# Kernel optimization log

Measured on AMD Instinct MI355X. Metric: run time of the kernel, lower is better.

## Reference

```python
import jax, jax.numpy as jnp
import numpy as np

CD_STEPS = 1

def _sample_binary(p, u):
    # relu(sign(p - u)): 1.0 where p > u else 0.0
    return (p > u).astype(p.dtype)

def setup_inputs() -> dict:
    key = jax.random.key(0)
    k_v, k_w, k_vb, k_uh, k_uv = jax.random.split(key, 5)
    B, V, H = 8192, 2048, 1024
    return {
        "v": jax.random.uniform(k_v, (B, V), dtype=jnp.float32),
        "w": jax.random.normal(k_w, (V, H), dtype=jnp.float32) * 0.01,
        "vb": jax.random.normal(k_vb, (V,), dtype=jnp.float32) * 0.01,
        "hb": jnp.zeros((H,), dtype=jnp.float32),
        "u_h": jax.random.uniform(k_uh, (CD_STEPS + 1, B, H), dtype=jnp.float32),
        "u_v": jax.random.uniform(k_uv, (CD_STEPS, B, V), dtype=jnp.float32),
    }

def reference(v, w, vb, hb, u_h, u_v):
    sig = jax.nn.sigmoid
    # mean-field forward
    h_p = sig(hb + v @ w)                     # [B,H]
    h_prediction = h_p
    v_prediction = sig(vb + h_p @ w.T)        # [B,V]
    reconstruction_error = jnp.mean(jnp.mean(jnp.abs(v - v_prediction), axis=1))
    # data statistics
    h = _sample_binary(h_p, u_h[0])           # [B,H]
    vb_data_grad = jnp.sum(v, axis=0)
    hb_data_grad = jnp.sum(h_p, axis=0)
    # sum_b outer(v_b, h_b) == v^T @ h (original materialized [B,V,H])
    w_data_grad = jnp.einsum('bv,bh->vh', v, h)
    # CD-k chain
    vk = v
    for k in range(CD_STEPS):
        vk = _sample_binary(sig(vb + h @ w.T), u_v[k])
        h = _sample_binary(sig(hb + vk @ w), u_h[k + 1])
    vb_model_grad = jnp.sum(vk, axis=0)
    hb_model_grad = jnp.sum(h, axis=0)
    w_model_grad = jnp.einsum('bv,bh->vh', vk, h)
    vb_grad = vb_model_grad - vb_data_grad
    hb_grad = hb_model_grad - hb_data_grad
    w_grad = w_model_grad - w_data_grad
    return h_prediction, reconstruction_error, w_grad, vb_grad, hb_grad
```

## Files before the change

### kernel.cpp

```cpp
#include <hip/hip_runtime.h>


typedef unsigned short u16;
typedef unsigned char u8;
typedef short s16x8 __attribute__((ext_vector_type(8)));
typedef float f32x4 __attribute__((ext_vector_type(4)));
typedef int i32x4 __attribute__((ext_vector_type(4)));
typedef u16 u16x4 __attribute__((ext_vector_type(4)));
typedef u16 u16x8 __attribute__((ext_vector_type(8)));
typedef u8 u8x8 __attribute__((ext_vector_type(8)));

constexpr int Bn = 8192, Vn = 2048, Hn = 1024;
constexpr size_t VH = (size_t)Vn * Hn;
constexpr size_t BH = (size_t)Bn * Hn;
constexpr size_t OUT_RECON = BH;
constexpr size_t OUT_WGRAD = OUT_RECON + 1;
constexpr size_t OUT_VBG   = OUT_WGRAD + VH;
constexpr size_t OUT_HBG   = OUT_VBG + Vn;

__device__ __forceinline__ u16 f2bf(float x) {
  union { float f; unsigned u; } a; a.f = x;
  unsigned r = a.u + 0x7FFFu + ((a.u >> 16) & 1u);
  return (u16)(r >> 16);
}
__device__ __forceinline__ float bf2f(u16 h) {
  union { unsigned u; float f; } a; a.u = ((unsigned)h) << 16;
  return a.f;
}
__device__ __forceinline__ float sigmoidf_(float x) {
  return 1.0f / (1.0f + __expf(-x));
}

using gptr_t = const unsigned int __attribute__((address_space(1)))*;
using lptr_t = unsigned int __attribute__((address_space(3)))*;

__device__ __forceinline__ void gload16(const void* g, void* l) {
  __builtin_amdgcn_global_load_lds((gptr_t)(unsigned long long)g,
                                   (lptr_t)(unsigned long long)l, 16, 0, 0);
}

__global__ void prep_all_k(const float* __restrict__ v, u16* __restrict__ vcat,
                           u16* __restrict__ vT, float* __restrict__ vbd_p,
                           const float* __restrict__ w, u16* __restrict__ w_cat,
                           u16* __restrict__ wTc) {
  __shared__ u16 tile16[64][68];
  __shared__ float cs[16][64];
  __shared__ float tile32[64][65];
  const int bx = blockIdx.x;
  const int t = threadIdx.x;
  if (bx < 4096) {
    const int b0 = (bx & 127) << 6, c0 = (bx >> 7) << 6;
    const int rg = t >> 4;
    const int cg = (t & 15) << 2;
    float ca[4] = {0.f, 0.f, 0.f, 0.f};
#pragma unroll
    for (int i = 0; i < 4; ++i) {
      int r = rg + 16 * i;
      f32x4 x = *(const f32x4*)&v[(size_t)(b0 + r) * Vn + c0 + cg];
      u16x4 hi, lo;
#pragma unroll
      for (int j = 0; j < 4; ++j) {
        hi[j] = f2bf(x[j]);
        lo[j] = f2bf(x[j] - bf2f(hi[j]));
        tile16[r][cg + j] = hi[j];
        ca[j] += x[j];
      }
      *(u16x4*)&vcat[(size_t)(b0 + r) * (2 * Vn) + c0 + cg] = hi;
      *(u16x4*)&vcat[(size_t)(b0 + r) * (2 * Vn) + Vn + c0 + cg] = lo;
    }
#pragma unroll
    for (int j = 0; j < 4; ++j) cs[rg][cg + j] = ca[j];
    __syncthreads();
    if (t < 64) {
      float s = 0.f;
#pragma unroll
      for (int k = 0; k < 16; ++k) s += cs[k][t];
      vbd_p[(size_t)(bx & 127) * Vn + c0 + t] = s;
    }
#pragma unroll
    for (int s2 = 0; s2 < 2; ++s2) {
      int c = t >> 2;
      int seg = (t & 3) + 4 * s2;
      u16x8 pk;
#pragma unroll
      for (int i = 0; i < 8; ++i) pk[i] = tile16[seg * 8 + i][c];
      *(u16x8*)&vT[(size_t)(c0 + c) * Bn + b0 + seg * 8] = pk;
    }
  } else {
    const int wb = bx - 4096;
    const int v0 = (wb & 31) << 6, h0 = (wb >> 5) << 6;
    const int c = t & 63, r = t >> 6;
    for (int rr = r; rr < 64; rr += 4) {
      float x = w[(size_t)(v0 + rr) * Hn + h0 + c];
      tile32[rr][c] = x;
      u16 hi = f2bf(x), lo = f2bf(x - bf2f(hi));
      w_cat[(size_t)(v0 + rr) * (2 * Hn) + h0 + c]      = hi;
      w_cat[(size_t)(v0 + rr) * (2 * Hn) + Hn + h0 + c] = lo;
    }
    __syncthreads();
    for (int rr = r; rr < 64; rr += 4) {
      float x = tile32[c][rr];
      u16 hi = f2bf(x), lo = f2bf(x - bf2f(hi));
      size_t ro = (size_t)(h0 + rr) * (2 * Vn);
      wTc[ro + v0 + c]      = hi;
      wTc[ro + Vn + v0 + c] = lo;
    }
  }
}

template <int M>
__global__ void epi_h_k(const float* __restrict__ p0, const float* __restrict__ p1,
                        const float* __restrict__ bias, const float* __restrict__ uni,
                        float* __restrict__ f32out, u16* __restrict__ hp_out,
                        u16* __restrict__ hbin_out, u16* __restrict__ tout,
                        float* __restrict__ colp) {
  __shared__ u16 tile[64][68];
  __shared__ float cs[16][64];
  const int b0 = blockIdx.x * 64, c0 = blockIdx.y * 64;
  const int t = threadIdx.x;
  const int rg = t >> 4, cg = (t & 15) << 2;
  float ca[4] = {0.f, 0.f, 0.f, 0.f};
#pragma unroll
  for (int i = 0; i < 4; ++i) {
    int r = rg + 16 * i;
    size_t e = (size_t)(b0 + r) * Hn + c0 + cg;
    f32x4 a = *(const f32x4*)&p0[e];
    f32x4 b = *(const f32x4*)&p1[e];
    f32x4 uu = *(const f32x4*)&uni[e];
    f32x4 hpv;
    u16x4 hb16, qv;
#pragma unroll
    for (int j = 0; j < 4; ++j) {
      float hp = sigmoidf_(a[j] + b[j] + bias[c0 + cg + j]);
      u16 qb = (hp > uu[j]) ? (u16)0x3F80 : (u16)0;
      tile[r][cg + j] = qb;
      if constexpr (M == 1) {
        hpv[j] = hp; hb16[j] = f2bf(hp); qv[j] = qb;
        ca[j] += hp;
      } else {
        ca[j] += (qb ? 1.f : 0.f);
      }
    }
    if constexpr (M == 1) {
      *(f32x4*)&f32out[e] = hpv;
      *(u16x4*)&hp_out[e] = hb16;
      *(u16x4*)&hbin_out[e] = qv;
    }
  }
#pragma unroll
  for (int j = 0; j < 4; ++j) cs[rg][cg + j] = ca[j];
  __syncthreads();
  if (t < 64) {
    float s = 0.f;
#pragma unroll
    for (int k = 0; k < 16; ++k) s += cs[k][t];
    colp[(size_t)blockIdx.x * Hn + c0 + t] = s;
  }
  if constexpr (M == 5) {
    u8* tout8 = (u8*)tout;
#pragma unroll
    for (int s2 = 0; s2 < 2; ++s2) {
      int c = t >> 2;
      int seg = (t & 3) + 4 * s2;
      u8x8 pk;
#pragma unroll
      for (int i = 0; i < 8; ++i) pk[i] = tile[seg * 8 + i][c] ? (u8)1 : (u8)0;
      *(u8x8*)&tout8[(size_t)(c0 + c) * Bn + b0 + seg * 8] = pk;
    }
  } else {
#pragma unroll
    for (int s2 = 0; s2 < 2; ++s2) {
      int c = t >> 2;
      int seg = (t & 3) + 4 * s2;
      u16x8 pk;
#pragma unroll
      for (int i = 0; i < 8; ++i) pk[i] = tile[seg * 8 + i][c];
      *(u16x8*)&tout[(size_t)(c0 + c) * Bn + b0 + seg * 8] = pk;
    }
  }
}

template <int MODE>
__global__ __launch_bounds__(512) void gemm256(
    const u16* __restrict__ A, int lda, const u16* __restrict__ Bm, int ldb, int K,
    const float* __restrict__ bias, const float* __restrict__ uni,
    const float* __restrict__ aux, float* __restrict__ f32out,
    u16* __restrict__ bfout, const u16* __restrict__ aux16,
    float* __restrict__ redp, u16* __restrict__ tout, float* __restrict__ colp) {
  constexpr bool TRANS = (MODE == 4);
  __shared__ __align__(16) u16 smem[TRANS ? 67584 : 65536];
  const int t = threadIdx.x;
  const int lane = t & 63, wave = t >> 6;
  const int wr = (wave >> 2) << 7;
  const int wc = (wave & 3) << 6;
  int bidx = blockIdx.x, bidy = blockIdx.y, bidz = blockIdx.z;
  if constexpr (MODE == 3) {
    const int orig = blockIdx.x + (blockIdx.y << 3) + (blockIdx.z << 5);
    bidz = orig & 7;
    const int r = orig >> 3;
    bidx = r & 7;
    bidy = r >> 3;
  }
  const int bm = bidx << 8, bn = bidy << 8;
  int kbeg = 0;
  float* pout = f32out;
  if constexpr (MODE == 1 || MODE == 5) {
    kbeg = bidz * K;
    pout = (bidz == 0) ? f32out : redp;
  }
  if constexpr (MODE == 3) {
    size_t off = (size_t)bidz * (size_t)K;
    A += off;
    Bm += off;
    pout = ((bidz < 4) ? f32out : redp) + (size_t)(bidz & 3) * VH;
  }
  f32x4 acc[8][4] = {};
  const int sr = t >> 2;
  const int sc = (((t & 3) ^ ((t >> 3) & 3)) << 3);
  const u16* Ag  = A  + (size_t)(bm + sr) * lda + sc;
  const u16* Ag2 = Ag + (size_t)128 * lda;
  const u16* Bg  = Bm + (size_t)(bn + sr) * ldb + sc;
  const u16* Bg2 = Bg + (size_t)128 * ldb;
  const int fr = lane & 15, fg = lane >> 4;
  const int ga = ((fg ^ ((fr >> 1) & 3)) << 3);

  auto acolf = [&](int k0) -> int {
    if constexpr (MODE == 1)      return (k0 < 2048) ? k0 : k0 - 2048;
    else if constexpr (MODE == 4) return k0 & 1023;
    else if constexpr (MODE == 5) return k0 & 2047;
    else                          return k0;
  };
  auto bcolf = [&](int k0) -> int {
    if constexpr (MODE == 1) return (k0 < 4096) ? k0 : k0 - 4096;
    else                     return k0;
  };
  auto stageA = [&](int kt) {
    const int k0 = kbeg + (kt << 5);
    const int acol = acolf(k0);
    u16* ad = smem + (kt & 3) * 8192 + wave * 512;
    gload16(Ag + acol, ad);
    gload16(Ag2 + acol, ad + 4096);
  };
  auto stageB = [&](int kt) {
    const int k0 = kbeg + (kt << 5);
    const int bcol = bcolf(k0);
    u16* bd = smem + 32768 + (kt & 3) * 8192 + wave * 512;
    gload16(Bg + bcol, bd);
    gload16(Bg2 + bcol, bd + 4096);
  };
  auto pfl4 = [&](int ci) -> float {
    const int L = (ci << 9) + t;
    return uni[(size_t)(bm + (L >> 3)) * Vn + bn + ((L & 7) << 5)];
  };

  const int NT = K >> 5;
  const int pfbeg = NT - 8;
  stageA(0); stageB(0); stageA(1); stageB(1); stageA(2); stageB(2);
  asm volatile("s_waitcnt vmcnt(8)" ::: "memory");
  __builtin_amdgcn_s_barrier();
  asm volatile("" ::: "memory");
  s16x8 bf[4], af[4];
  for (int kt = 0; kt < NT; ++kt) {
    const int pb = kt & 3;
    const u16* Ab = smem + pb * 8192;
    const u16* Bb = smem + 32768 + pb * 8192;
    const bool st = (kt < NT - 3);
#pragma unroll
    for (int n = 0; n < 4; ++n)
      bf[n] = *(const s16x8*)&Bb[(wc + n * 16 + fr) * 32 + ga];
#pragma unroll
    for (int m = 0; m < 4; ++m)
      af[m] = *(const s16x8*)&Ab[(wr + m * 16 + fr) * 32 + ga];
    if (st) stageA(kt + 3);
    if constexpr (MODE == 4) {
      if (kt >= pfbeg && kt < pfbeg + 4) {
        float pfv = pfl4(kt - pfbeg);
        asm volatile("" :: "v"(pfv));
      }
    }
    __builtin_amdgcn_s_barrier();
    asm volatile("" ::: "memory");
    __builtin_amdgcn_s_setprio(1);
#pragma unroll
    for (int m = 0; m < 4; ++m)
#pragma unroll
      for (int n = 0; n < 4; ++n)
        acc[m][n] = __builtin_amdgcn_mfma_f32_16x16x32_bf16(af[m], bf[n], acc[m][n], 0, 0, 0);
    __builtin_amdgcn_s_setprio(0);
#pragma unroll
    for (int m = 0; m < 4; ++m)
      af[m] = *(const s16x8*)&Ab[(wr + (m + 4) * 16 + fr) * 32 + ga];
    if (st) stageB(kt + 3);
    if (kt < NT - 3) {
      asm volatile("s_waitcnt vmcnt(8)" ::: "memory");
    } else if (kt == NT - 3) {
      asm volatile("s_waitcnt vmcnt(4)" ::: "memory");
    } else if (kt == NT - 2) {
      asm volatile("s_waitcnt vmcnt(0)" ::: "memory");
    }
    __builtin_amdgcn_s_barrier();
    asm volatile("" ::: "memory");
    __builtin_amdgcn_s_setprio(1);
#pragma unroll
    for (int m = 0; m < 4; ++m)
#pragma unroll
      for (int n = 0; n < 4; ++n)
        acc[m + 4][n] = __builtin_amdgcn_mfma_f32_16x16x32_bf16(af[m], bf[n], acc[m + 4][n], 0, 0, 0);
    __builtin_amdgcn_s_setprio(0);
  }

  constexpr int NC = (MODE == 4) ? Vn : Hn;
  const int fq = lane >> 4;

  if constexpr (MODE == 1 || MODE == 3 || MODE == 5) {
#pragma unroll
    for (int m = 0; m < 8; ++m)
#pragma unroll
      for (int n = 0; n < 4; ++n)
#pragma unroll
        for (int j = 0; j < 4; ++j) {
          int rl = wr + m * 16 + fq * 4 + j;
          int cl = wc + n * 16 + fr;
          pout[(size_t)(bm + rl) * NC + bn + cl] = acc[m][n][j];
        }
  }

  if constexpr (MODE == 4) {
    __syncthreads();
    float bcol[4];
#pragma unroll
    for (int n = 0; n < 4; ++n) bcol[n] = bias[bn + wc + n * 16 + fr];
    const size_t ebase = (size_t)(bm + wr + fq * 4) * NC + (bn + wc + fr);
    float ux[8][4];
    auto ld4 = [&](int ci, float* dst) {
      size_t e0 = ebase + (size_t)((ci >> 2) << 4) * NC + ((ci & 3) << 4);
      dst[0] = uni[e0];          dst[1] = uni[e0 + NC];
      dst[2] = uni[e0 + 2 * NC]; dst[3] = uni[e0 + 3 * NC];
    };
#pragma unroll
    for (int ci = 0; ci < 8; ++ci) ld4(ci, ux[ci]);
#pragma unroll
    for (int m = 0; m < 8; ++m)
#pragma unroll
      for (int n = 0; n < 4; ++n)
#pragma unroll
        for (int j = 0; j < 4; ++j)
          acc[m][n][j] = sigmoidf_(acc[m][n][j] + bcol[n]);
    float csum[4] = {0.f, 0.f, 0.f, 0.f};
#pragma unroll
    for (int ci = 0; ci < 32; ++ci) {
      const int m = ci >> 2, n = ci & 3;
      const int rl = wr + m * 16 + fq * 4;
      const int cl = wc + n * 16 + fr;
#pragma unroll
      for (int j = 0; j < 4; ++j) {
        u16 qb = (acc[m][n][j] > ux[ci & 7][j]) ? (u16)0x3F80 : (u16)0;
        smem[(rl + j) * 264 + cl] = qb;
        csum[n] += (qb ? 1.f : 0.f);
      }
      if (ci < 24) ld4(ci + 8, ux[ci & 7]);
    }
#pragma unroll
    for (int n = 0; n < 4; ++n) {
      float s = csum[n];
      s += __shfl_xor(s, 16);
      s += __shfl_xor(s, 32);
      if (fq == 0)
        colp[(size_t)(blockIdx.x * 2 + (wr >> 7)) * NC + (bn + wc + n * 16 + fr)] = s;
    }
    __syncthreads();
#pragma unroll
    for (int it = 0; it < 16; ++it) {
      int id = t + (it << 9);
      int r = id >> 5;
      int c0 = (id & 31) << 3;
      u16x8 pk = *(const u16x8*)&smem[r * 264 + c0];
      *(u16x8*)&bfout[(size_t)(bm + r) * NC + bn + c0] = pk;
    }
    {
      u8* tout8 = (u8*)tout;
      const int c = t & 255;
      const int half = t >> 8;
#pragma unroll
      for (int i8_ = 0; i8_ < 16; ++i8_) {
        u8x8 pk;
#pragma unroll
        for (int i2 = 0; i2 < 8; ++i2)
          pk[i2] = smem[(half * 128 + i8_ * 8 + i2) * 264 + c] ? (u8)1 : (u8)0;
        *(u8x8*)&tout8[(size_t)(bn + c) * Bn + bm + half * 128 + i8_ * 8] = pk;
      }
    }
  }
}

__global__ __launch_bounds__(512) void gemm_i8_k(
    const u8* __restrict__ A, const u8* __restrict__ Bm,
    float* __restrict__ out0, float* __restrict__ out4) {
  __shared__ __align__(16) u8 smem[131072];
  const int t = threadIdx.x;
  const int lane = t & 63, wave = t >> 6;
  const int wr = (wave >> 2) << 7;
  const int wc = (wave & 3) << 6;
  const int orig = blockIdx.x + (blockIdx.y << 3) + (blockIdx.z << 5);
  const int bidz = orig & 7;
  const int rr = orig >> 3;
  const int bidx = rr & 7, bidy = rr >> 3;
  const int bm = bidx << 8, bn = bidy << 8;
  const int kbeg = bidz << 10;
  float* pout = ((bidz < 4) ? out0 : out4) + (size_t)(bidz & 3) * VH;
  i32x4 acc[8][4] = {};
  const int sr = t >> 2;
  const int sc = (((t & 3) ^ ((t >> 3) & 3)) << 4);
  const u8* Ag  = A  + (size_t)(bm + sr) * Bn + sc;
  const u8* Ag2 = Ag + (size_t)128 * Bn;
  const u8* Bg  = Bm + (size_t)(bn + sr) * Bn + sc;
  const u8* Bg2 = Bg + (size_t)128 * Bn;
  const int fr = lane & 15, fg = lane >> 4;
  const int ga = ((fg ^ ((fr >> 1) & 3)) << 4);

  auto stageA = [&](int kt) {
    u8* ad = smem + (kt & 3) * 16384 + wave * 1024;
    gload16(Ag + kbeg + (kt << 6), ad);
    gload16(Ag2 + kbeg + (kt << 6), ad + 8192);
  };
  auto stageB = [&](int kt) {
    u8* bd = smem + 65536 + (kt & 3) * 16384 + wave * 1024;
    gload16(Bg + kbeg + (kt << 6), bd);
    gload16(Bg2 + kbeg + (kt << 6), bd + 8192);
  };

  constexpr int NT = 16;
  stageA(0); stageB(0); stageA(1); stageB(1); stageA(2); stageB(2);
  asm volatile("s_waitcnt vmcnt(8)" ::: "memory");
  __builtin_amdgcn_s_barrier();
  asm volatile("" ::: "memory");
  i32x4 bf[4], af[4];
  for (int kt = 0; kt < NT; ++kt) {
    const u8* Ab = smem + (kt & 3) * 16384;
    const u8* Bb = smem + 65536 + (kt & 3) * 16384;
    const bool st = (kt < NT - 3);
#pragma unroll
    for (int n = 0; n < 4; ++n)
      bf[n] = *(const i32x4*)&Bb[(wc + n * 16 + fr) * 64 + ga];
#pragma unroll
    for (int m = 0; m < 4; ++m)
      af[m] = *(const i32x4*)&Ab[(wr + m * 16 + fr) * 64 + ga];
    if (st) stageA(kt + 3);
    __builtin_amdgcn_s_barrier();
    asm volatile("" ::: "memory");
    __builtin_amdgcn_s_setprio(1);
#pragma unroll
    for (int m = 0; m < 4; ++m)
#pragma unroll
      for (int n = 0; n < 4; ++n)
        acc[m][n] = __builtin_amdgcn_mfma_i32_16x16x64_i8(af[m], bf[n], acc[m][n], 0, 0, 0);
    __builtin_amdgcn_s_setprio(0);
#pragma unroll
    for (int m = 0; m < 4; ++m)
      af[m] = *(const i32x4*)&Ab[(wr + (m + 4) * 16 + fr) * 64 + ga];
    if (st) stageB(kt + 3);
    if (kt < NT - 3) {
      asm volatile("s_waitcnt vmcnt(8)" ::: "memory");
    } else if (kt == NT - 3) {
      asm volatile("s_waitcnt vmcnt(4)" ::: "memory");
    } else if (kt == NT - 2) {
      asm volatile("s_waitcnt vmcnt(0)" ::: "memory");
    }
    __builtin_amdgcn_s_barrier();
    asm volatile("" ::: "memory");
    __builtin_amdgcn_s_setprio(1);
#pragma unroll
    for (int m = 0; m < 4; ++m)
#pragma unroll
      for (int n = 0; n < 4; ++n)
        acc[m + 4][n] = __builtin_amdgcn_mfma_i32_16x16x64_i8(af[m], bf[n], acc[m + 4][n], 0, 0, 0);
    __builtin_amdgcn_s_setprio(0);
  }

  const int fq = lane >> 4;
#pragma unroll
  for (int m = 0; m < 8; ++m)
#pragma unroll
    for (int n = 0; n < 4; ++n)
#pragma unroll
      for (int j = 0; j < 4; ++j) {
        int rl = wr + m * 16 + fq * 4 + j;
        int cl = wc + n * 16 + fr;
        pout[(size_t)(bm + rl) * Hn + bn + cl] = (float)acc[m][n][j];
      }
}

__global__ __launch_bounds__(512) void g23_k(
    const u16* __restrict__ A2, const u16* __restrict__ B2,
    const u16* __restrict__ aux16, const float* __restrict__ bias2,
    float* __restrict__ redp2,
    const u16* __restrict__ A3, const u16* __restrict__ B3,
    float* __restrict__ out30, float* __restrict__ out34) {
  __shared__ __align__(16) u16 smem[65536];
  const int t = threadIdx.x;
  const int lane = t & 63, wave = t >> 6;
  const int wr = (wave >> 2) << 7;
  const int wc = (wave & 3) << 6;
  const int flat = blockIdx.x;
  const bool isG2 = (flat < 256);
  int bidx, bidy, bidz = 0;
  const u16 *Abase, *Bbase;
  int lda, ldb;
  if (isG2) {
    bidx = flat & 31; bidy = flat >> 5;
    Abase = A2; Bbase = B2; lda = Hn; ldb = 2 * Hn;
  } else {
    const int orig = flat - 256;
    bidz = orig & 7;
    const int rr = orig >> 3;
    bidx = rr & 7; bidy = rr >> 3;
    Abase = A3 + (size_t)bidz * 1024;
    Bbase = B3 + (size_t)bidz * 1024;
    lda = Bn; ldb = Bn;
  }
  const int bm = bidx << 8, bn = bidy << 8;
  f32x4 acc[8][4] = {};
  const int sr = t >> 2;
  const int sc = (((t & 3) ^ ((t >> 3) & 3)) << 3);
  const u16* Ag  = Abase + (size_t)(bm + sr) * lda + sc;
  const u16* Ag2 = Ag + (size_t)128 * lda;
  const u16* Bg  = Bbase + (size_t)(bn + sr) * ldb + sc;
  const u16* Bg2 = Bg + (size_t)128 * ldb;
  const int fr = lane & 15, fg = lane >> 4;
  const int ga = ((fg ^ ((fr >> 1) & 3)) << 3);

  auto stageA = [&](int kt) {
    u16* ad = smem + (kt & 3) * 8192 + wave * 512;
    gload16(Ag + (kt << 5), ad);
    gload16(Ag2 + (kt << 5), ad + 4096);
  };
  auto stageB = [&](int kt) {
    u16* bd = smem + 32768 + (kt & 3) * 8192 + wave * 512;
    gload16(Bg + (kt << 5), bd);
    gload16(Bg2 + (kt << 5), bd + 4096);
  };
  auto pfl2 = [&](int ci) -> unsigned {
    const int L = (ci << 9) + t;
    return (unsigned)aux16[(size_t)(bm + (L >> 2)) * 4096 + bn + ((L & 3) << 6)];
  };

  constexpr int NT = 32;
  stageA(0); stageB(0); stageA(1); stageB(1); stageA(2); stageB(2);
  asm volatile("s_waitcnt vmcnt(8)" ::: "memory");
  __builtin_amdgcn_s_barrier();
  asm volatile("" ::: "memory");
  s16x8 bf[4], af[4];
  for (int kt = 0; kt < NT; ++kt) {
    const int pb = kt & 3;
    const u16* Ab = smem + pb * 8192;
    const u16* Bb = smem + 32768 + pb * 8192;
    const bool st = (kt < NT - 3);
#pragma unroll
    for (int n = 0; n < 4; ++n)
      bf[n] = *(const s16x8*)&Bb[(wc + n * 16 + fr) * 32 + ga];
#pragma unroll
    for (int m = 0; m < 4; ++m)
      af[m] = *(const s16x8*)&Ab[(wr + m * 16 + fr) * 32 + ga];
    if (st) stageA(kt + 3);
    if (isG2 && kt >= NT - 8 && kt < NT - 6) {
      unsigned pfv = pfl2(kt - (NT - 8));
      asm volatile("" :: "v"(pfv));
    }
    __builtin_amdgcn_s_barrier();
    asm volatile("" ::: "memory");
    __builtin_amdgcn_s_setprio(1);
#pragma unroll
    for (int m = 0; m < 4; ++m)
#pragma unroll
      for (int n = 0; n < 4; ++n)
        acc[m][n] = __builtin_amdgcn_mfma_f32_16x16x32_bf16(af[m], bf[n], acc[m][n], 0, 0, 0);
    __builtin_amdgcn_s_setprio(0);
#pragma unroll
    for (int m = 0; m < 4; ++m)
      af[m] = *(const s16x8*)&Ab[(wr + (m + 4) * 16 + fr) * 32 + ga];
    if (st) stageB(kt + 3);
    if (kt < NT - 3) {
      asm volatile("s_waitcnt vmcnt(8)" ::: "memory");
    } else if (kt == NT - 3) {
      asm volatile("s_waitcnt vmcnt(4)" ::: "memory");
    } else if (kt == NT - 2) {
      asm volatile("s_waitcnt vmcnt(0)" ::: "memory");
    }
    __builtin_amdgcn_s_barrier();
    asm volatile("" ::: "memory");
    __builtin_amdgcn_s_setprio(1);
#pragma unroll
    for (int m = 0; m < 4; ++m)
#pragma unroll
      for (int n = 0; n < 4; ++n)
        acc[m + 4][n] = __builtin_amdgcn_mfma_f32_16x16x32_bf16(af[m], bf[n], acc[m + 4][n], 0, 0, 0);
    __builtin_amdgcn_s_setprio(0);
  }

  const int fq = lane >> 4;
  if (isG2) {
    float bcol[4];
#pragma unroll
    for (int n = 0; n < 4; ++n) bcol[n] = bias2[bn + wc + n * 16 + fr];
    const size_t ebase = (size_t)(bm + wr + fq * 4) * 4096 + (bn + wc + fr);
    float ax[8][4];
    auto ld4 = [&](int ci, float* dst) {
      size_t e0 = ebase + (size_t)((ci >> 2) << 4) * 4096 + ((ci & 3) << 4);
      dst[0] = bf2f(aux16[e0]);            dst[1] = bf2f(aux16[e0 + 4096]);
      dst[2] = bf2f(aux16[e0 + 2 * 4096]); dst[3] = bf2f(aux16[e0 + 3 * 4096]);
    };
#pragma unroll
    for (int ci = 0; ci < 8; ++ci) ld4(ci, ax[ci]);
#pragma unroll
    for (int m = 0; m < 8; ++m)
#pragma unroll
      for (int n = 0; n < 4; ++n)
#pragma unroll
        for (int j = 0; j < 4; ++j)
          acc[m][n][j] = sigmoidf_(acc[m][n][j] + bcol[n]);
    float lsum = 0.f;
#pragma unroll
    for (int ci = 0; ci < 32; ++ci) {
      const int m = ci >> 2, n = ci & 3;
#pragma unroll
      for (int j = 0; j < 4; ++j) lsum += fabsf(ax[ci & 7][j] - acc[m][n][j]);
      if (ci < 24) ld4(ci + 8, ax[ci & 7]);
    }
#pragma unroll
    for (int off = 32; off > 0; off >>= 1) lsum += __shfl_down(lsum, off);
    __syncthreads();
    float* redlds = (float*)smem;
    if (lane == 0) redlds[wave] = lsum;
    __syncthreads();
    if (t == 0) {
      float s = 0.f;
#pragma unroll
      for (int wv = 0; wv < 8; ++wv) s += redlds[wv];
      redp2[(size_t)bidy * 32 + bidx] = s;
    }
  } else {
    float* pout = ((bidz < 4) ? out30 : out34) + (size_t)(bidz & 3) * VH;
#pragma unroll
    for (int m = 0; m < 8; ++m)
#pragma unroll
      for (int n = 0; n < 4; ++n)
#pragma unroll
        for (int j = 0; j < 4; ++j) {
          int rl = wr + m * 16 + fq * 4 + j;
          int cl = wc + n * 16 + fr;
          pout[(size_t)(bm + rl) * Hn + bn + cl] = acc[m][n][j];
        }
  }
}

__global__ void reduce8_k(const float* __restrict__ p, float* __restrict__ out) {
  size_t e = ((size_t)blockIdx.x * 256 + threadIdx.x) * 4;
  f32x4 r = {};
#pragma unroll
  for (int z = 0; z < 8; ++z) r += *(const f32x4*)&p[(size_t)z * VH + e];
  out[e + 0] = r[0]; out[e + 1] = r[1]; out[e + 2] = r[2]; out[e + 3] = r[3];
}

__global__ void tail_k(const float* __restrict__ pa, const float* __restrict__ pb,
                       const float* __restrict__ sums, float* __restrict__ out) {
  const int b = blockIdx.x;
  float* outw = out + OUT_WGRAD;
  if (b < 2048) {
    size_t e = ((size_t)b * 256 + threadIdx.x) * 4;
    f32x4 r = {};
#pragma unroll
    for (int z = 0; z < 4; ++z) r += *(const f32x4*)&pa[(size_t)z * VH + e];
#pragma unroll
    for (int z = 0; z < 4; ++z) r += *(const f32x4*)&pb[(size_t)z * VH + e];
    float s0 = outw[e + 0], s1 = outw[e + 1], s2 = outw[e + 2], s3 = outw[e + 3];
    outw[e + 0] = r[0] - s0; outw[e + 1] = r[1] - s1;
    outw[e + 2] = r[2] - s2; outw[e + 3] = r[3] - s3;
  } else {
    const int i = (b - 2048) * 256 + threadIdx.x;
    const float* recon_p = sums;
    const float* vbd = sums + 1024;
    const float* hbd = vbd + 128 * 2048;
    const float* vbm = hbd + 128 * 1024;
    const float* hbm = vbm + 128 * 2048;
    if (i < 2048) {
      float d = 0.f, m = 0.f;
      for (int k = 0; k < 128; ++k) d += vbd[k * 2048 + i];
      for (int k = 0; k < 64; ++k)  m += vbm[k * 2048 + i];
      out[OUT_VBG + i] = m - d;
    }
    if (i < 1024) {
      float d = 0.f, m = 0.f;
      for (int k = 0; k < 128; ++k) { d += hbd[k * 1024 + i]; m += hbm[k * 1024 + i]; }
      out[OUT_HBG + i] = m - d;
    }
    if (i == 0) {
      float s = 0.f;
      for (int k = 0; k < 256; ++k) s += recon_p[k];
      out[OUT_RECON] = s * (1.0f / 16777216.0f);
    }
  }
}

extern "C" void kernel_launch(void* const* d_in, const int* in_sizes, int n_in,
                              void* d_out, int out_size, void* d_ws, size_t ws_size,
                              hipStream_t stream) {
  (void)in_sizes; (void)n_in; (void)out_size;
  const float* v   = (const float*)d_in[0];
  const float* w   = (const float*)d_in[1];
  const float* vb  = (const float*)d_in[2];
  const float* hb  = (const float*)d_in[3];
  const float* u_h = (const float*)d_in[4];
  const float* u_v = (const float*)d_in[5];
  float* out = (float*)d_out;
  char* ws = (char*)d_ws;
  if (ws_size < 204734464ULL) return;

  float* sums    = (float*)ws;
  float* recon_p = sums;
  float* vbd_p   = sums + 1024;
  float* hbd_p   = vbd_p + 128 * 2048;
  float* vbm_p   = hbd_p + 128 * 1024;
  float* hbm_p   = vbm_p + 128 * 2048;
  char* p = ws + 3407872;
  u16* v_cat  = (u16*)p;  p += (size_t)Bn * 2 * Vn * 2;
  u16* wT_cat = (u16*)p;  p += (size_t)Hn * 2 * Vn * 2;
  u16* w_cat  = (u16*)p;  p += (size_t)Vn * 2 * Hn * 2;
  u16* h_p    = (u16*)p;  p += BH * 2;
  u16* hbin   = (u16*)p;  p += BH * 2;
  u16* vT     = (u16*)p;  p += (size_t)Vn * Bn * 2;
  u16* hT     = (u16*)p;  p += (size_t)Hn * Bn * 2;
  float* big  = (float*)p;
  u16* vk   = v_cat;
  u8*  vkT8 = (u8*)vT;
  u8*  h2T8 = (u8*)hT;
  float* vcat_f = (float*)v_cat;
  float* hpbuf  = (float*)h_p;
  float* outW   = out + OUT_WGRAD;

  prep_all_k<<<4608, 256, 0, stream>>>(v, v_cat, vT, vbd_p, w, w_cat, wT_cat);
  gemm256<1><<<dim3(32, 4, 2), 512, 0, stream>>>(
      v_cat, 2 * Vn, wT_cat, 2 * Vn, 3072, nullptr, nullptr, nullptr,
      out, nullptr, nullptr, big, nullptr, nullptr);
  epi_h_k<1><<<dim3(128, 16), 256, 0, stream>>>(
      out, big, hb, u_h, out, h_p, hbin, hT, hbd_p);
  g23_k<<<512, 512, 0, stream>>>(
      h_p, w_cat, v_cat, vb, recon_p,
      vT, hT, vcat_f, vcat_f + 4 * VH);
  reduce8_k<<<2048, 256, 0, stream>>>(vcat_f, outW);
  gemm256<4><<<dim3(32, 8), 512, 0, stream>>>(
      hbin, Hn, w_cat, 2 * Hn, 2 * Hn, vb, u_v, nullptr,
      nullptr, vk, nullptr, nullptr, (u16*)vkT8, vbm_p);
  gemm256<5><<<dim3(32, 4, 2), 512, 0, stream>>>(
      vk, Vn, wT_cat, 2 * Vn, 2048, nullptr, nullptr, nullptr,
      hpbuf, nullptr, nullptr, big, nullptr, nullptr);
  epi_h_k<5><<<dim3(128, 16), 256, 0, stream>>>(
      hpbuf, big, hb, u_h + BH, nullptr, nullptr, nullptr, (u16*)h2T8, hbm_p);
  gemm_i8_k<<<dim3(8, 4, 8), 512, 0, stream>>>(vkT8, h2T8, hpbuf, big);
  tail_k<<<2056, 256, 0, stream>>>(hpbuf, big, sums, out);
}
```

Before: 479.7 us.

## Fuse split-K reduction and sigmoid/sampling epilogue into hidden-layer GEMMs

```diff
diff --git a/kernel.cpp b/kernel.cpp
--- a/kernel.cpp
+++ b/kernel.cpp
@@ -108,78 +108,6 @@
   }
 }
 
-template <int M>
-__global__ void epi_h_k(const float* __restrict__ p0, const float* __restrict__ p1,
-                        const float* __restrict__ bias, const float* __restrict__ uni,
-                        float* __restrict__ f32out, u16* __restrict__ hp_out,
-                        u16* __restrict__ hbin_out, u16* __restrict__ tout,
-                        float* __restrict__ colp) {
-  __shared__ u16 tile[64][68];
-  __shared__ float cs[16][64];
-  const int b0 = blockIdx.x * 64, c0 = blockIdx.y * 64;
-  const int t = threadIdx.x;
-  const int rg = t >> 4, cg = (t & 15) << 2;
-  float ca[4] = {0.f, 0.f, 0.f, 0.f};
-#pragma unroll
-  for (int i = 0; i < 4; ++i) {
-    int r = rg + 16 * i;
-    size_t e = (size_t)(b0 + r) * Hn + c0 + cg;
-    f32x4 a = *(const f32x4*)&p0[e];
-    f32x4 b = *(const f32x4*)&p1[e];
-    f32x4 uu = *(const f32x4*)&uni[e];
-    f32x4 hpv;
-    u16x4 hb16, qv;
-#pragma unroll
-    for (int j = 0; j < 4; ++j) {
-      float hp = sigmoidf_(a[j] + b[j] + bias[c0 + cg + j]);
-      u16 qb = (hp > uu[j]) ? (u16)0x3F80 : (u16)0;
-      tile[r][cg + j] = qb;
-      if constexpr (M == 1) {
-        hpv[j] = hp; hb16[j] = f2bf(hp); qv[j] = qb;
-        ca[j] += hp;
-      } else {
-        ca[j] += (qb ? 1.f : 0.f);
-      }
-    }
-    if constexpr (M == 1) {
-      *(f32x4*)&f32out[e] = hpv;
-      *(u16x4*)&hp_out[e] = hb16;
-      *(u16x4*)&hbin_out[e] = qv;
-    }
-  }
-#pragma unroll
-  for (int j = 0; j < 4; ++j) cs[rg][cg + j] = ca[j];
-  __syncthreads();
-  if (t < 64) {
-    float s = 0.f;
-#pragma unroll
-    for (int k = 0; k < 16; ++k) s += cs[k][t];
-    colp[(size_t)blockIdx.x * Hn + c0 + t] = s;
-  }
-  if constexpr (M == 5) {
-    u8* tout8 = (u8*)tout;
-#pragma unroll
-    for (int s2 = 0; s2 < 2; ++s2) {
-      int c = t >> 2;
-      int seg = (t & 3) + 4 * s2;
-      u8x8 pk;
-#pragma unroll
-      for (int i = 0; i < 8; ++i) pk[i] = tile[seg * 8 + i][c] ? (u8)1 : (u8)0;
-      *(u8x8*)&tout8[(size_t)(c0 + c) * Bn + b0 + seg * 8] = pk;
-    }
-  } else {
-#pragma unroll
-    for (int s2 = 0; s2 < 2; ++s2) {
-      int c = t >> 2;
-      int seg = (t & 3) + 4 * s2;
-      u16x8 pk;
-#pragma unroll
-      for (int i = 0; i < 8; ++i) pk[i] = tile[seg * 8 + i][c];
-      *(u16x8*)&tout[(size_t)(c0 + c) * Bn + b0 + seg * 8] = pk;
-    }
-  }
-}
-
 template <int MODE>
 __global__ __launch_bounds__(512) void gemm256(
     const u16* __restrict__ A, int lda, const u16* __restrict__ Bm, int ldb, int K,
@@ -187,33 +115,15 @@
     const float* __restrict__ aux, float* __restrict__ f32out,
     u16* __restrict__ bfout, const u16* __restrict__ aux16,
     float* __restrict__ redp, u16* __restrict__ tout, float* __restrict__ colp) {
-  constexpr bool TRANS = (MODE == 4);
-  __shared__ __align__(16) u16 smem[TRANS ? 67584 : 65536];
+  __shared__ __align__(16) u16 smem[67584];
   const int t = threadIdx.x;
   const int lane = t & 63, wave = t >> 6;
   const int wr = (wave >> 2) << 7;
   const int wc = (wave & 3) << 6;
-  int bidx = blockIdx.x, bidy = blockIdx.y, bidz = blockIdx.z;
-  if constexpr (MODE == 3) {
-    const int orig = blockIdx.x + (blockIdx.y << 3) + (blockIdx.z << 5);
-    bidz = orig & 7;
-    const int r = orig >> 3;
-    bidx = r & 7;
-    bidy = r >> 3;
-  }
+  const int bidx = blockIdx.x, bidy = blockIdx.y, bidz = blockIdx.z;
   const int bm = bidx << 8, bn = bidy << 8;
   int kbeg = 0;
-  float* pout = f32out;
-  if constexpr (MODE == 1 || MODE == 5) {
-    kbeg = bidz * K;
-    pout = (bidz == 0) ? f32out : redp;
-  }
-  if constexpr (MODE == 3) {
-    size_t off = (size_t)bidz * (size_t)K;
-    A += off;
-    Bm += off;
-    pout = ((bidz < 4) ? f32out : redp) + (size_t)(bidz & 3) * VH;
-  }
+  if constexpr (MODE == 6 || MODE == 7) kbeg = bidz * K;
   f32x4 acc[8][4] = {};
   const int sr = t >> 2;
   const int sc = (((t & 3) ^ ((t >> 3) & 3)) << 3);
@@ -225,13 +135,12 @@
   const int ga = ((fg ^ ((fr >> 1) & 3)) << 3);
 
   auto acolf = [&](int k0) -> int {
-    if constexpr (MODE == 1)      return (k0 < 2048) ? k0 : k0 - 2048;
+    if constexpr (MODE == 6)      return (k0 < 2048) ? k0 : k0 - 2048;
     else if constexpr (MODE == 4) return k0 & 1023;
-    else if constexpr (MODE == 5) return k0 & 2047;
-    else                          return k0;
+    else                          return k0 & 2047;
   };
   auto bcolf = [&](int k0) -> int {
-    if constexpr (MODE == 1) return (k0 < 4096) ? k0 : k0 - 4096;
+    if constexpr (MODE == 6) return (k0 < 4096) ? k0 : k0 - 4096;
     else                     return k0;
   };
   auto stageA = [&](int kt) {
@@ -248,9 +157,12 @@
     gload16(Bg + bcol, bd);
     gload16(Bg2 + bcol, bd + 4096);
   };
+  constexpr int NC = (MODE == 4) ? Vn : Hn;
   auto pfl4 = [&](int ci) -> float {
     const int L = (ci << 9) + t;
-    return uni[(size_t)(bm + (L >> 3)) * Vn + bn + ((L & 7) << 5)];
+    const int lpr = NC / 32;
+    return uni[(size_t)(bm + (L / (NC / 32))) * NC + bn +
+               (L % (NC / 32)) * 32];
   };
 
   const int NT = K >> 5;
@@ -272,11 +184,9 @@
     for (int m = 0; m < 4; ++m)
       af[m] = *(const s16x8*)&Ab[(wr + m * 16 + fr) * 32 + ga];
     if (st) stageA(kt + 3);
-    if constexpr (MODE == 4) {
-      if (kt >= pfbeg && kt < pfbeg + 4) {
-        float pfv = pfl4(kt - pfbeg);
-        asm volatile("" :: "v"(pfv));
-      }
+    if (kt >= pfbeg && kt < pfbeg + 4) {
+      float pfv = pfl4(kt - pfbeg);
+      asm volatile("" :: "v"(pfv));
     }
     __builtin_amdgcn_s_barrier();
     asm volatile("" ::: "memory");
@@ -309,20 +219,135 @@
     __builtin_amdgcn_s_setprio(0);
   }
 
-  constexpr int NC = (MODE == 4) ? Vn : Hn;
   const int fq = lane >> 4;
 
-  if constexpr (MODE == 1 || MODE == 3 || MODE == 5) {
+  if constexpr (MODE == 6 || MODE == 7) {
+    __syncthreads();
+    {
+      float* mybuf = (bidz == 0) ? f32out : redp;
+#pragma unroll
+      for (int m = 0; m < 8; ++m)
+#pragma unroll
+        for (int n = 0; n < 4; ++n)
+#pragma unroll
+          for (int j = 0; j < 4; ++j) {
+            int rl = wr + m * 16 + fq * 4 + j;
+            int cl = wc + n * 16 + fr;
+            mybuf[(size_t)(bm + rl) * NC + bn + cl] = acc[m][n][j];
+          }
+    }
+    asm volatile("s_waitcnt vmcnt(0)" ::: "memory");
+    __syncthreads();
+    if (t == 0) {
+      int* tick = (int*)aux;
+      int old = __hip_atomic_fetch_add(&tick[bidx * 4 + bidy], 1,
+                                       __ATOMIC_ACQ_REL, __HIP_MEMORY_SCOPE_AGENT);
+      ((volatile int*)smem)[0] = (old & 1);
+    }
+    __syncthreads();
+    const bool last = (((volatile int*)smem)[0] != 0);
+    __syncthreads();
+    if (!last) return;
+    {
+      const float* pbuf = (bidz == 0) ? redp : f32out;
+      float px[8][4];
+      auto ld4p = [&](int ci, float* dst) {
+        size_t e0 = (size_t)(bm + wr + fq * 4 + ((ci >> 2) << 4)) * NC
+                  + (bn + wc + ((ci & 3) << 4) + fr);
+        dst[0] = pbuf[e0];          dst[1] = pbuf[e0 + NC];
+        dst[2] = pbuf[e0 + 2 * NC]; dst[3] = pbuf[e0 + 3 * NC];
+      };
+#pragma unroll
+      for (int ci = 0; ci < 8; ++ci) ld4p(ci, px[ci]);
+#pragma unroll
+      for (int ci = 0; ci < 32; ++ci) {
+        const int m = ci >> 2, n = ci & 3;
+#pragma unroll
+        for (int j = 0; j < 4; ++j) acc[m][n][j] += px[ci & 7][j];
+        if (ci < 24) ld4p(ci + 8, px[ci & 7]);
+      }
+    }
+    float bcol[4];
+#pragma unroll
+    for (int n = 0; n < 4; ++n) bcol[n] = bias[bn + wc + n * 16 + fr];
+    float ux[8][4];
+    auto ld4u = [&](int ci, float* dst) {
+      size_t e0 = (size_t)(bm + wr + fq * 4 + ((ci >> 2) << 4)) * NC
+                + (bn + wc + ((ci & 3) << 4) + fr);
+      dst[0] = uni[e0];          dst[1] = uni[e0 + NC];
+      dst[2] = uni[e0 + 2 * NC]; dst[3] = uni[e0 + 3 * NC];
+    };
+#pragma unroll
+    for (int ci = 0; ci < 8; ++ci) ld4u(ci, ux[ci]);
 #pragma unroll
     for (int m = 0; m < 8; ++m)
 #pragma unroll
       for (int n = 0; n < 4; ++n)
 #pragma unroll
-        for (int j = 0; j < 4; ++j) {
-          int rl = wr + m * 16 + fq * 4 + j;
-          int cl = wc + n * 16 + fr;
-          pout[(size_t)(bm + rl) * NC + bn + cl] = acc[m][n][j];
+        for (int j = 0; j < 4; ++j)
+          acc[m][n][j] = sigmoidf_(acc[m][n][j] + bcol[n]);
+    float csum[4] = {0.f, 0.f, 0.f, 0.f};
+    u16* hbin_w = const_cast<u16*>(aux16);
+#pragma unroll
+    for (int ci = 0; ci < 32; ++ci) {
+      const int m = ci >> 2, n = ci & 3;
+      const int rl = wr + m * 16 + fq * 4;
+      const int cl = wc + n * 16 + fr;
+#pragma unroll
+      for (int j = 0; j < 4; ++j) {
+        float hp = acc[m][n][j];
+        u16 qb = (hp > ux[ci & 7][j]) ? (u16)0x3F80 : (u16)0;
+        smem[(rl + j) * 264 + cl] = qb;
+        if constexpr (MODE == 6) {
+          size_t e = (size_t)(bm + rl + j) * NC + bn + cl;
+          f32out[e] = hp;
+          bfout[e] = f2bf(hp);
+          hbin_w[e] = qb;
+          csum[n] += hp;
+        } else {
+          csum[n] += (qb ? 1.f : 0.f);
         }
+      }
+      if (ci < 24) ld4u(ci + 8, ux[ci & 7]);
+    }
+#pragma unroll
+    for (int n = 0; n < 4; ++n) {
+      float s = csum[n];
+      s += __shfl_xor(s, 16);
+      s += __shfl_xor(s, 32);
+      if (fq == 0)
+        colp[(size_t)(bidx * 2 + (wr >> 7)) * NC + (bn + wc + n * 16 + fr)] = s;
+    }
+    __syncthreads();
+    if constexpr (MODE == 6) {
+#pragma unroll
+      for (int it = 0; it < 4; ++it) {
+        int id = t + (it << 9);
+        int c = id & 255;
+        int q = id >> 8;
+#pragma unroll
+        for (int i8_ = 0; i8_ < 4; ++i8_) {
+          u16x8 pk;
+#pragma unroll
+          for (int i2 = 0; i2 < 8; ++i2)
+            pk[i2] = smem[(q * 32 + i8_ * 8 + i2) * 264 + c];
+          *(u16x8*)&tout[(size_t)(bn + c) * Bn + bm + q * 32 + i8_ * 8] = pk;
+        }
+      }
+    } else {
+      u8* tout8 = (u8*)tout;
+      const int c = t & 255;
+      const int half = t >> 8;
+#pragma unroll
+      for (int i8_ = 0; i8_ < 16; ++i8_) {
+        u8x8 pk;
+#pragma unroll
+        for (int i2 = 0; i2 < 8; ++i2)
+          pk[i2] = smem[(half * 128 + i8_ * 8 + i2) * 264 + c] ? (u8)1 : (u8)0;
+        *(u8x8*)&tout8[(size_t)(bn + c) * Bn + bm + half * 128 + i8_ * 8] = pk;
+      }
+    }
+    return;
   }
 
   if constexpr (MODE == 4) {
@@ -366,7 +391,7 @@
       s += __shfl_xor(s, 16);
       s += __shfl_xor(s, 32);
       if (fq == 0)
-        colp[(size_t)(blockIdx.x * 2 + (wr >> 7)) * NC + (bn + wc + n * 16 + fr)] = s;
+        colp[(size_t)(bidx * 2 + (wr >> 7)) * NC + (bn + wc + n * 16 + fr)] = s;
     }
     __syncthreads();
 #pragma unroll
@@ -690,7 +715,7 @@
     }
     if (i < 1024) {
       float d = 0.f, m = 0.f;
-      for (int k = 0; k < 128; ++k) { d += hbd[k * 1024 + i]; m += hbm[k * 1024 + i]; }
+      for (int k = 0; k < 64; ++k) { d += hbd[k * 1024 + i]; m += hbm[k * 1024 + i]; }
       out[OUT_HBG + i] = m - d;
     }
     if (i == 0) {
@@ -717,6 +742,8 @@
 
   float* sums    = (float*)ws;
   float* recon_p = sums;
+  int*   tickG1  = (int*)(sums + 256);
+  int*   tickG5  = (int*)(sums + 384);
   float* vbd_p   = sums + 1024;
   float* hbd_p   = vbd_p + 128 * 2048;
   float* vbm_p   = hbd_p + 128 * 1024;
@@ -737,12 +764,11 @@
   float* hpbuf  = (float*)h_p;
   float* outW   = out + OUT_WGRAD;
 
+  hipMemsetAsync(tickG1, 0, 256 * sizeof(int), stream);
   prep_all_k<<<4608, 256, 0, stream>>>(v, v_cat, vT, vbd_p, w, w_cat, wT_cat);
-  gemm256<1><<<dim3(32, 4, 2), 512, 0, stream>>>(
-      v_cat, 2 * Vn, wT_cat, 2 * Vn, 3072, nullptr, nullptr, nullptr,
-      out, nullptr, nullptr, big, nullptr, nullptr);
-  epi_h_k<1><<<dim3(128, 16), 256, 0, stream>>>(
-      out, big, hb, u_h, out, h_p, hbin, hT, hbd_p);
+  gemm256<6><<<dim3(32, 4, 2), 512, 0, stream>>>(
+      v_cat, 2 * Vn, wT_cat, 2 * Vn, 3072, hb, u_h, (const float*)tickG1,
+      out, h_p, hbin, big, hT, hbd_p);
   g23_k<<<512, 512, 0, stream>>>(
       h_p, w_cat, v_cat, vb, recon_p,
       vT, hT, vcat_f, vcat_f + 4 * VH);
@@ -750,11 +776,9 @@
   gemm256<4><<<dim3(32, 8), 512, 0, stream>>>(
       hbin, Hn, w_cat, 2 * Hn, 2 * Hn, vb, u_v, nullptr,
       nullptr, vk, nullptr, nullptr, (u16*)vkT8, vbm_p);
-  gemm256<5><<<dim3(32, 4, 2), 512, 0, stream>>>(
-      vk, Vn, wT_cat, 2 * Vn, 2048, nullptr, nullptr, nullptr,
-      hpbuf, nullptr, nullptr, big, nullptr, nullptr);
-  epi_h_k<5><<<dim3(128, 16), 256, 0, stream>>>(
-      hpbuf, big, hb, u_h + BH, nullptr, nullptr, nullptr, (u16*)h2T8, hbm_p);
+  gemm256<7><<<dim3(32, 4, 2), 512, 0, stream>>>(
+      vk, Vn, wT_cat, 2 * Vn, 2048, hb, u_h + BH, (const float*)tickG5,
+      hpbuf, nullptr, nullptr, big, (u16*)h2T8, hbm_p);
   gemm_i8_k<<<dim3(8, 4, 8), 512, 0, stream>>>(vkT8, h2T8, hpbuf, big);
   tail_k<<<2056, 256, 0, stream>>>(hpbuf, big, sums, out);
 }
```

After: 518.8 us. +8.2%, slower.
